# Optimization experiments

Measured on AMD Instinct MI355X. Metric: run time of the kernel, lower is better.

The kernel has to match this reference:

```python
import jax, jax.numpy as jnp
import numpy as np

E = 7          # num experts
K = 1          # top-k
R = 8          # LoRA rank
C = 768        # channels
DEPTHS = [[0, 1, 2, 3], [4, 5], [6]]   # deep2idx
EPS = float(np.finfo(np.float64).eps)  # np.finfo(float).eps in the torch code


def setup_inputs() -> dict:
    key = jax.random.key(0)
    k0, k1, k2, k3 = jax.random.split(key, 4)
    B, N = 8, 2048
    x = jax.random.normal(k0, (B, N, C), jnp.float32)
    w_gate = jax.random.normal(k1, (C, E), jnp.float32) * 0.02
    # Lora_a weight is [r, C] per expert (nn.Linear(in, d).weight); Lora_b is [C, r].
    Wa = jax.random.normal(k2, (3, E, R, C), jnp.float32) * 0.02
    Wb = jax.random.normal(k3, (3, E, C, R), jnp.float32) * 0.02
    return {"x": x, "w_gate": w_gate, "Wa": Wa, "Wb": Wb}


def _cv_squared(v):
    # torch .var() default is unbiased (ddof=1)
    return jnp.var(v, ddof=1) / (jnp.mean(v) ** 2 + 1e-10)


def _gating(xf, w_gate):
    # eval-mode noisy_top_k_gating (no noise): top-k of clean logits, softmax over top-k
    logits = xf @ w_gate                                   # [T, E]
    top_vals, top_idx = jax.lax.top_k(logits, K + 1)        # m = k+1
    gate_vals = jax.nn.softmax(top_vals[:, :K], axis=1)     # [T, K]
    rows = jnp.arange(xf.shape[0])[:, None]
    gates = jnp.zeros_like(logits).at[rows, top_idx[:, :K]].set(gate_vals)
    return gates                                            # [T, E]


def _expert_outputs(xf, Wa_a, Wb_a):
    # All-expert LoRA outputs (dense-masked equivalent of SparseDispatcher):
    # lora_i(x) = (x @ Wa_i^T) @ Wb_i^T  -- rank-8 grouped GEMMs
    h = jnp.einsum('erc,tc->etr', Wa_a, xf)                 # [E, T, R]
    lora = jnp.einsum('edr,etr->etd', Wb_a, h)              # [E, T, C]
    outs = [None] * E
    for j in DEPTHS[0]:
        outs[j] = lora[j]
    prev = DEPTHS[0]
    for lvl in (1, 2):  # hierarchical: own LoRA + mean of previous-level expert outputs
        prev_mean = sum(outs[j] for j in prev) / float(len(prev))
        for i in DEPTHS[lvl]:
            outs[i] = lora[i] + prev_mean
        prev = DEPTHS[lvl]
    return jnp.stack(outs)                                  # [E, T, C]


def reference(x, w_gate, Wa, Wb):
    B, N, Cc = x.shape
    xf = x.reshape(B * N, Cc)                               # token-level gating path
    gates = _gating(xf, w_gate)                             # [T, E]
    importance = gates.sum(0)
    load = (gates > 0).sum(0).astype(jnp.float32)           # _gates_to_load
    loss = _cv_squared(importance) + _cv_squared(load)
    ys = []
    for a in range(3):  # q, k, v adapters
        outs = _expert_outputs(xf, Wa[a], Wb[a])            # [E, T, C]
        # SparseDispatcher.combine: log( index_add( exp(expert_out) * gate ) )
        comb = jnp.einsum('te,etc->tc', gates, jnp.exp(outs))
        comb = jnp.where(comb == 0, EPS, comb)
        ys.append(jnp.log(comb))
    return jnp.stack(ys), loss                              # ([3, T, C], scalar)
```

## Files before the change

### kernel.cpp

```cpp
#include <hip/hip_runtime.h>

#define C_DIM 768


__global__ __launch_bounds__(256) void transpose_wa(
    const float* __restrict__ wa, const float* __restrict__ wg,
    float4* __restrict__ waT4) {
  const int g = blockIdx.x * 256 + threadIdx.x;
  const int o = g % 192, k4 = g / 192;
  float4 v = make_float4(0.f, 0.f, 0.f, 0.f);
  if (o < 168) {
    v = *(const float4*)(wa + (size_t)o * C_DIM + k4 * 4);
  } else if (o < 175) {
    const int e = o - 168;
    v.x = wg[(k4 * 4 + 0) * 7 + e];
    v.y = wg[(k4 * 4 + 1) * 7 + e];
    v.z = wg[(k4 * 4 + 2) * 7 + e];
    v.w = wg[(k4 * 4 + 3) * 7 + e];
  }
  waT4[g] = v;
}

__global__ __launch_bounds__(256) void transpose_wb(
    const float* __restrict__ wb, float4* __restrict__ wbT4) {
  const int g = blockIdx.x * 256 + threadIdx.x;
  const int c4 = g % 192, ak = g / 192;
  const int a = ak / 56, k = ak - a * 56;
  const int e = k >> 3, r = k & 7;
  const float* s = wb + ((size_t)(a * 7 + e) * C_DIM + c4 * 4) * 8 + r;
  wbT4[g] = make_float4(s[0], s[8], s[16], s[24]);
}

__global__ __launch_bounds__(256, 2) void moe_main(
    const float* __restrict__ x, const float4* __restrict__ waT4,
    const float4* __restrict__ wbT4, float* __restrict__ out,
    unsigned int* __restrict__ counts, int T) {
  __shared__ float xs[4][2][8][64];
  __shared__ float hsT[168][36];

  const int tid = threadIdx.x;
  const int w = tid >> 6, lane = tid & 63;
  const int half = lane >> 5, l5 = lane & 31;
  const int t0 = blockIdx.x * 32;
  const int tb = w * 8;

  float acc1[4][6];
  #pragma unroll
  for (int tl = 0; tl < 4; ++tl)
    #pragma unroll
    for (int m = 0; m < 6; ++m) acc1[tl][m] = 0.f;

  const int xt = lane >> 3, xc = (lane & 7) * 8;
  const float* xbase = x + (size_t)(t0 + tb + xt) * C_DIM + xc;
  const float4* wa_l = waT4 + l5;

  float4 xr0 = *(const float4*)(xbase);
  float4 xr1 = *(const float4*)(xbase + 4);
  *(float4*)&xs[w][0][xt][xc]     = xr0;
  *(float4*)&xs[w][0][xt][xc + 4] = xr1;
  xr0 = *(const float4*)(xbase + 64);
  xr1 = *(const float4*)(xbase + 68);

  float4 wv[2][6];
  #pragma unroll
  for (int m = 0; m < 6; ++m) wv[0][m] = wa_l[32 * m];
  #pragma unroll
  for (int m = 0; m < 6; ++m) wv[1][m] = wa_l[192 + 32 * m];

  #pragma unroll 1
  for (int ch = 0; ch < 12; ++ch) {
    if (ch < 11) {
      *(float4*)&xs[w][(ch + 1) & 1][xt][xc]     = xr0;
      *(float4*)&xs[w][(ch + 1) & 1][xt][xc + 4] = xr1;
      if (ch < 10) {
        xr0 = *(const float4*)(xbase + (ch + 2) * 64);
        xr1 = *(const float4*)(xbase + (ch + 2) * 64 + 4);
      }
    }
    const int buf = ch & 1;
    #pragma unroll
    for (int kk = 0; kk < 16; ++kk) {
      const int p = kk & 1;
      float4 xv[4];
      #pragma unroll
      for (int tl = 0; tl < 4; ++tl)
        xv[tl] = *(const float4*)&xs[w][buf][half * 4 + tl][kk * 4];
      #pragma unroll
      for (int m = 0; m < 6; ++m) {
        const float4 wvv = wv[p][m];
        #pragma unroll
        for (int tl = 0; tl < 4; ++tl) {
          float s = acc1[tl][m];
          s = fmaf(xv[tl].x, wvv.x, s);
          s = fmaf(xv[tl].y, wvv.y, s);
          s = fmaf(xv[tl].z, wvv.z, s);
          s = fmaf(xv[tl].w, wvv.w, s);
          acc1[tl][m] = s;
        }
      }
      int gn = ch * 16 + kk + 2;
      gn = gn > 191 ? 191 : gn;
      #pragma unroll
      for (int m = 0; m < 6; ++m) wv[p][m] = wa_l[(size_t)gn * 192 + 32 * m];
    }
  }

  int be[4];
  #pragma unroll
  for (int tl = 0; tl < 4; ++tl) {
    float best = __shfl(acc1[tl][5], (lane & 32) + 8);
    int b = 0;
    #pragma unroll
    for (int e = 1; e < 7; ++e) {
      const float lv = __shfl(acc1[tl][5], (lane & 32) + 8 + e);
      if (lv > best) { best = lv; b = e; }
    }
    be[tl] = b;
  }
  if (l5 == 0) {
    #pragma unroll
    for (int tl = 0; tl < 4; ++tl) atomicAdd(&counts[be[tl]], 1u);
  }

  #pragma unroll
  for (int tl = 0; tl < 4; ++tl) {
    const int b = be[tl];
    const int tcol = tb + half * 4 + tl;
    #pragma unroll
    for (int m = 0; m < 6; ++m) {
      const int o = l5 + 32 * m;
      if (o < 168) {
        const int e = (o % 56) >> 3;
        float co = (e == b) ? 1.f : 0.f;
        if (b >= 4 && e < 4) co += 0.25f;
        if (b == 6 && (e == 4 || e == 5)) co += 0.5f;
        hsT[o][tcol] = acc1[tl][m] * co;
      }
    }
  }

  const float4* wb_l = wbT4 + lane;
  float4 u[2][3], hb[2][2];
  #pragma unroll
  for (int cc = 0; cc < 3; ++cc) {
    u[0][cc] = wb_l[64 * cc];
    u[1][cc] = wb_l[192 + 64 * cc];
  }
  hb[0][0] = *(const float4*)&hsT[0][tb];
  hb[0][1] = *(const float4*)&hsT[0][tb + 4];
  hb[1][0] = *(const float4*)&hsT[1][tb];
  hb[1][1] = *(const float4*)&hsT[1][tb + 4];

  #pragma unroll 1
  for (int a = 0; a < 3; ++a) {
    float4 acc2[3][8];
    #pragma unroll
    for (int cc = 0; cc < 3; ++cc)
      #pragma unroll
      for (int t = 0; t < 8; ++t) acc2[cc][t] = make_float4(0.f, 0.f, 0.f, 0.f);

    #pragma unroll 4
    for (int kq = 0; kq < 56; ++kq) {
      const int o = a * 56 + kq;
      const int p = kq & 1;
      const float hv[8] = {hb[p][0].x, hb[p][0].y, hb[p][0].z, hb[p][0].w,
                           hb[p][1].x, hb[p][1].y, hb[p][1].z, hb[p][1].w};
      const float4 w0 = u[p][0], w1 = u[p][1], w2 = u[p][2];
      #pragma unroll
      for (int t = 0; t < 8; ++t) {
        const float s = hv[t];
        acc2[0][t].x = fmaf(w0.x, s, acc2[0][t].x);
        acc2[0][t].y = fmaf(w0.y, s, acc2[0][t].y);
        acc2[0][t].z = fmaf(w0.z, s, acc2[0][t].z);
        acc2[0][t].w = fmaf(w0.w, s, acc2[0][t].w);
        acc2[1][t].x = fmaf(w1.x, s, acc2[1][t].x);
        acc2[1][t].y = fmaf(w1.y, s, acc2[1][t].y);
        acc2[1][t].z = fmaf(w1.z, s, acc2[1][t].z);
        acc2[1][t].w = fmaf(w1.w, s, acc2[1][t].w);
        acc2[2][t].x = fmaf(w2.x, s, acc2[2][t].x);
        acc2[2][t].y = fmaf(w2.y, s, acc2[2][t].y);
        acc2[2][t].z = fmaf(w2.z, s, acc2[2][t].z);
        acc2[2][t].w = fmaf(w2.w, s, acc2[2][t].w);
      }
      int on = o + 2;
      on = on > 167 ? 167 : on;
      #pragma unroll
      for (int cc = 0; cc < 3; ++cc) u[p][cc] = wb_l[(size_t)on * 192 + 64 * cc];
      hb[p][0] = *(const float4*)&hsT[on][tb];
      hb[p][1] = *(const float4*)&hsT[on][tb + 4];
    }

    #pragma unroll
    for (int cc = 0; cc < 3; ++cc)
      #pragma unroll
      for (int t = 0; t < 8; ++t)
        *(float4*)(out + ((size_t)a * T + t0 + tb + t) * C_DIM + cc * 256 + lane * 4)
            = acc2[cc][t];
  }
}

__global__ void loss_k(const unsigned int* __restrict__ counts,
                       float* __restrict__ out, int T) {
  if (threadIdx.x == 0) {
    float c[7], mean = 0.f;
    #pragma unroll
    for (int e = 0; e < 7; ++e) { c[e] = (float)counts[e]; mean += c[e]; }
    mean *= (1.f / 7.f);
    float var = 0.f;
    #pragma unroll
    for (int e = 0; e < 7; ++e) { const float d = c[e] - mean; var += d * d; }
    var *= (1.f / 6.f);
    out[(size_t)3 * T * C_DIM] = 2.f * (var / (mean * mean + 1e-10f));
  }
}

extern "C" void kernel_launch(void* const* d_in, const int* in_sizes, int n_in,
                              void* d_out, int out_size, void* d_ws, size_t ws_size,
                              hipStream_t stream) {
  const float* x  = (const float*)d_in[0];
  const float* wg = (const float*)d_in[1];
  const float* Wa = (const float*)d_in[2];
  const float* Wb = (const float*)d_in[3];
  float* out = (float*)d_out;

  unsigned int* counts = (unsigned int*)d_ws;
  float4* waT4 = (float4*)((char*)d_ws + 1024);
  float4* wbT4 = (float4*)((char*)d_ws + 590848);

  const int T = in_sizes[0] / C_DIM;

  hipMemsetAsync(counts, 0, 8 * sizeof(unsigned int), stream);
  transpose_wa<<<dim3(144), dim3(256), 0, stream>>>(Wa, wg, waT4);
  transpose_wb<<<dim3(126), dim3(256), 0, stream>>>(Wb, wbT4);
  moe_main<<<dim3(T / 32), dim3(256), 0, stream>>>(x, waT4, wbT4, out, counts, T);
  loss_k<<<dim3(1), dim3(64), 0, stream>>>(counts, out, T);
}
```

Before: 417.1 us.

## Stage gate/LoRA weights through double-buffered LDS shared across warps

The main kernel now loads LoRA-A/gate and LoRA-B weight chunks cooperatively into double-buffered shared memory, along with the x tile. All four warps reuse those chunks instead of each warp streaming the weights from global memory into registers. The B-phase is restructured into 21 chunks of 8 rows, with accumulator reset and output stores every 7 chunks. The two weight transpose kernels are merged into one launch. The cost is a block barrier per chunk and much larger LDS use (about 81KB per block), which may limit the kernel to one resident block per CU.

```diff
diff --git a/kernel.cpp b/kernel.cpp
--- a/kernel.cpp
+++ b/kernel.cpp
@@ -3,39 +3,41 @@
 #define C_DIM 768
 
 
-__global__ __launch_bounds__(256) void transpose_wa(
+__global__ __launch_bounds__(256) void transpose_w(
     const float* __restrict__ wa, const float* __restrict__ wg,
-    float4* __restrict__ waT4) {
-  const int g = blockIdx.x * 256 + threadIdx.x;
-  const int o = g % 192, k4 = g / 192;
-  float4 v = make_float4(0.f, 0.f, 0.f, 0.f);
-  if (o < 168) {
-    v = *(const float4*)(wa + (size_t)o * C_DIM + k4 * 4);
-  } else if (o < 175) {
-    const int e = o - 168;
-    v.x = wg[(k4 * 4 + 0) * 7 + e];
-    v.y = wg[(k4 * 4 + 1) * 7 + e];
-    v.z = wg[(k4 * 4 + 2) * 7 + e];
-    v.w = wg[(k4 * 4 + 3) * 7 + e];
-  }
-  waT4[g] = v;
-}
-
-__global__ __launch_bounds__(256) void transpose_wb(
-    const float* __restrict__ wb, float4* __restrict__ wbT4) {
-  const int g = blockIdx.x * 256 + threadIdx.x;
-  const int c4 = g % 192, ak = g / 192;
-  const int a = ak / 56, k = ak - a * 56;
-  const int e = k >> 3, r = k & 7;
-  const float* s = wb + ((size_t)(a * 7 + e) * C_DIM + c4 * 4) * 8 + r;
-  wbT4[g] = make_float4(s[0], s[8], s[16], s[24]);
+    const float* __restrict__ wb,
+    float4* __restrict__ waT4, float4* __restrict__ wbT4) {
+  const int b = blockIdx.x;
+  if (b < 144) {
+    const int g = b * 256 + threadIdx.x;
+    const int o = g % 192, k4 = g / 192;
+    float4 v = make_float4(0.f, 0.f, 0.f, 0.f);
+    if (o < 168) {
+      v = *(const float4*)(wa + (size_t)o * C_DIM + k4 * 4);
+    } else if (o < 175) {
+      const int e = o - 168;
+      v.x = wg[(k4 * 4 + 0) * 7 + e];
+      v.y = wg[(k4 * 4 + 1) * 7 + e];
+      v.z = wg[(k4 * 4 + 2) * 7 + e];
+      v.w = wg[(k4 * 4 + 3) * 7 + e];
+    }
+    waT4[g] = v;
+  } else {
+    const int g = (b - 144) * 256 + threadIdx.x;
+    const int c4 = g % 192, ak = g / 192;
+    const int a = ak / 56, k = ak - a * 56;
+    const int e = k >> 3, r = k & 7;
+    const float* s = wb + ((size_t)(a * 7 + e) * C_DIM + c4 * 4) * 8 + r;
+    wbT4[g] = make_float4(s[0], s[8], s[16], s[24]);
+  }
 }
 
 __global__ __launch_bounds__(256, 2) void moe_main(
     const float* __restrict__ x, const float4* __restrict__ waT4,
     const float4* __restrict__ wbT4, float* __restrict__ out,
     unsigned int* __restrict__ counts, int T) {
-  __shared__ float xs[4][2][8][64];
+  __shared__ float4 wbuf[2][1536];
+  __shared__ float4 xbuf[2][32][8];
   __shared__ float hsT[168][36];
 
   const int tid = threadIdx.x;
@@ -44,65 +46,61 @@
   const int t0 = blockIdx.x * 32;
   const int tb = w * 8;
 
+  const int sxt = tid >> 3, sxs = tid & 7;
+  const float4* x4 = (const float4*)x;
+  const size_t xrow = (size_t)(t0 + sxt) * 192 + sxs;
+
+  float4 stw[6], stx;
+  #pragma unroll
+  for (int j = 0; j < 6; ++j) stw[j] = waT4[tid + j * 256];
+  stx = x4[xrow];
+  #pragma unroll
+  for (int j = 0; j < 6; ++j) wbuf[0][tid + j * 256] = stw[j];
+  xbuf[0][sxt][sxs] = stx;
+  __syncthreads();
+
   float acc1[4][6];
   #pragma unroll
   for (int tl = 0; tl < 4; ++tl)
     #pragma unroll
     for (int m = 0; m < 6; ++m) acc1[tl][m] = 0.f;
 
-  const int xt = lane >> 3, xc = (lane & 7) * 8;
-  const float* xbase = x + (size_t)(t0 + tb + xt) * C_DIM + xc;
-  const float4* wa_l = waT4 + l5;
-
-  float4 xr0 = *(const float4*)(xbase);
-  float4 xr1 = *(const float4*)(xbase + 4);
-  *(float4*)&xs[w][0][xt][xc]     = xr0;
-  *(float4*)&xs[w][0][xt][xc + 4] = xr1;
-  xr0 = *(const float4*)(xbase + 64);
-  xr1 = *(const float4*)(xbase + 68);
-
-  float4 wv[2][6];
-  #pragma unroll
-  for (int m = 0; m < 6; ++m) wv[0][m] = wa_l[32 * m];
-  #pragma unroll
-  for (int m = 0; m < 6; ++m) wv[1][m] = wa_l[192 + 32 * m];
-
   #pragma unroll 1
-  for (int ch = 0; ch < 12; ++ch) {
-    if (ch < 11) {
-      *(float4*)&xs[w][(ch + 1) & 1][xt][xc]     = xr0;
-      *(float4*)&xs[w][(ch + 1) & 1][xt][xc + 4] = xr1;
-      if (ch < 10) {
-        xr0 = *(const float4*)(xbase + (ch + 2) * 64);
-        xr1 = *(const float4*)(xbase + (ch + 2) * 64 + 4);
-      }
-    }
-    const int buf = ch & 1;
-    #pragma unroll
-    for (int kk = 0; kk < 16; ++kk) {
-      const int p = kk & 1;
+  for (int c = 0; c < 24; ++c) {
+    const int cb = c & 1, nb = cb ^ 1;
+    if (c < 23) {
+      #pragma unroll
+      for (int j = 0; j < 6; ++j)
+        stw[j] = waT4[(size_t)(c + 1) * 1536 + tid + j * 256];
+      stx = x4[xrow + (size_t)(c + 1) * 8];
+    } else {
+      #pragma unroll
+      for (int j = 0; j < 6; ++j) stw[j] = wbT4[tid + j * 256];
+    }
+    #pragma unroll
+    for (int s = 0; s < 8; ++s) {
       float4 xv[4];
       #pragma unroll
       for (int tl = 0; tl < 4; ++tl)
-        xv[tl] = *(const float4*)&xs[w][buf][half * 4 + tl][kk * 4];
+        xv[tl] = xbuf[cb][tb + half * 4 + tl][s];
       #pragma unroll
       for (int m = 0; m < 6; ++m) {
-        const float4 wvv = wv[p][m];
+        const float4 wv = wbuf[cb][s * 192 + l5 + 32 * m];
         #pragma unroll
         for (int tl = 0; tl < 4; ++tl) {
-          float s = acc1[tl][m];
-          s = fmaf(xv[tl].x, wvv.x, s);
-          s = fmaf(xv[tl].y, wvv.y, s);
-          s = fmaf(xv[tl].z, wvv.z, s);
-          s = fmaf(xv[tl].w, wvv.w, s);
-          acc1[tl][m] = s;
+          float v = acc1[tl][m];
+          v = fmaf(xv[tl].x, wv.x, v);
+          v = fmaf(xv[tl].y, wv.y, v);
+          v = fmaf(xv[tl].z, wv.z, v);
+          v = fmaf(xv[tl].w, wv.w, v);
+          acc1[tl][m] = v;
         }
       }
-      int gn = ch * 16 + kk + 2;
-      gn = gn > 191 ? 191 : gn;
-      #pragma unroll
-      for (int m = 0; m < 6; ++m) wv[p][m] = wa_l[(size_t)gn * 192 + 32 * m];
-    }
+    }
+    #pragma unroll
+    for (int j = 0; j < 6; ++j) wbuf[nb][tid + j * 256] = stw[j];
+    if (c < 23) xbuf[nb][sxt][sxs] = stx;
+    __syncthreads();
   }
 
   int be[4];
@@ -139,33 +137,34 @@
     }
   }
 
-  const float4* wb_l = wbT4 + lane;
-  float4 u[2][3], hb[2][2];
-  #pragma unroll
-  for (int cc = 0; cc < 3; ++cc) {
-    u[0][cc] = wb_l[64 * cc];
-    u[1][cc] = wb_l[192 + 64 * cc];
-  }
-  hb[0][0] = *(const float4*)&hsT[0][tb];
-  hb[0][1] = *(const float4*)&hsT[0][tb + 4];
-  hb[1][0] = *(const float4*)&hsT[1][tb];
-  hb[1][1] = *(const float4*)&hsT[1][tb + 4];
+  float4 acc2[3][8];
+  float4* out4 = (float4*)out;
+  int a = 0, rc = 0;
 
   #pragma unroll 1
-  for (int a = 0; a < 3; ++a) {
-    float4 acc2[3][8];
-    #pragma unroll
-    for (int cc = 0; cc < 3; ++cc)
-      #pragma unroll
-      for (int t = 0; t < 8; ++t) acc2[cc][t] = make_float4(0.f, 0.f, 0.f, 0.f);
-
-    #pragma unroll 4
-    for (int kq = 0; kq < 56; ++kq) {
-      const int o = a * 56 + kq;
-      const int p = kq & 1;
-      const float hv[8] = {hb[p][0].x, hb[p][0].y, hb[p][0].z, hb[p][0].w,
-                           hb[p][1].x, hb[p][1].y, hb[p][1].z, hb[p][1].w};
-      const float4 w0 = u[p][0], w1 = u[p][1], w2 = u[p][2];
+  for (int d = 0; d < 21; ++d) {
+    const int cb = d & 1, nb = cb ^ 1;
+    if (d < 20) {
+      #pragma unroll
+      for (int j = 0; j < 6; ++j)
+        stw[j] = wbT4[(size_t)(d + 1) * 1536 + tid + j * 256];
+    }
+    if (rc == 0) {
+      #pragma unroll
+      for (int cc = 0; cc < 3; ++cc)
+        #pragma unroll
+        for (int t = 0; t < 8; ++t) acc2[cc][t] = make_float4(0.f, 0.f, 0.f, 0.f);
+    }
+    const int ob = a * 56 + rc * 8;
+    #pragma unroll
+    for (int q = 0; q < 8; ++q) {
+      const float4 hq0 = *(const float4*)&hsT[ob + q][tb];
+      const float4 hq1 = *(const float4*)&hsT[ob + q][tb + 4];
+      const float hv[8] = {hq0.x, hq0.y, hq0.z, hq0.w,
+                           hq1.x, hq1.y, hq1.z, hq1.w};
+      const float4 w0 = wbuf[cb][q * 192 + lane];
+      const float4 w1 = wbuf[cb][q * 192 + lane + 64];
+      const float4 w2 = wbuf[cb][q * 192 + lane + 128];
       #pragma unroll
       for (int t = 0; t < 8; ++t) {
         const float s = hv[t];
@@ -182,20 +181,22 @@
         acc2[2][t].z = fmaf(w2.z, s, acc2[2][t].z);
         acc2[2][t].w = fmaf(w2.w, s, acc2[2][t].w);
       }
-      int on = o + 2;
-      on = on > 167 ? 167 : on;
-      #pragma unroll
-      for (int cc = 0; cc < 3; ++cc) u[p][cc] = wb_l[(size_t)on * 192 + 64 * cc];
-      hb[p][0] = *(const float4*)&hsT[on][tb];
-      hb[p][1] = *(const float4*)&hsT[on][tb + 4];
-    }
-
-    #pragma unroll
-    for (int cc = 0; cc < 3; ++cc)
-      #pragma unroll
-      for (int t = 0; t < 8; ++t)
-        *(float4*)(out + ((size_t)a * T + t0 + tb + t) * C_DIM + cc * 256 + lane * 4)
-            = acc2[cc][t];
+    }
+    if (rc == 6) {
+      #pragma unroll
+      for (int cc = 0; cc < 3; ++cc)
+        #pragma unroll
+        for (int t = 0; t < 8; ++t)
+          out4[((size_t)a * T + t0 + tb + t) * 192 + cc * 64 + lane] = acc2[cc][t];
+      ++a; rc = 0;
+    } else {
+      ++rc;
+    }
+    if (d < 20) {
+      #pragma unroll
+      for (int j = 0; j < 6; ++j) wbuf[nb][tid + j * 256] = stw[j];
+      __syncthreads();
+    }
   }
 }
 
@@ -230,8 +231,7 @@
   const int T = in_sizes[0] / C_DIM;
 
   hipMemsetAsync(counts, 0, 8 * sizeof(unsigned int), stream);
-  transpose_wa<<<dim3(144), dim3(256), 0, stream>>>(Wa, wg, waT4);
-  transpose_wb<<<dim3(126), dim3(256), 0, stream>>>(Wb, wbT4);
+  transpose_w<<<dim3(270), dim3(256), 0, stream>>>(Wa, wg, Wb, waT4, wbT4);
   moe_main<<<dim3(T / 32), dim3(256), 0, stream>>>(x, waT4, wbT4, out, counts, T);
   loss_k<<<dim3(1), dim3(64), 0, stream>>>(counts, out, T);
 }
```

New measurement: 904.1 us. 2.17x slower.
